# Performance work log

Measured on AMD Instinct MI355X. Metric: run time of the kernel, lower is better.

## Reference

```python
import jax, jax.numpy as jnp
import numpy as np

WINDOW = 32


def _dilate(mask, iters=5):
    # scipy binary_dilation with default cross structure, `iters` iterations
    m = mask.copy()
    for _ in range(iters):
        d = m.copy()
        d[1:, :] |= m[:-1, :]
        d[:-1, :] |= m[1:, :]
        d[:, 1:] |= m[:, :-1]
        d[:, :-1] |= m[:, 1:]
        m = d
    return m


def _label8(mask):
    # skimage measure.label, default 8-connectivity, via min-label propagation
    h, w = mask.shape
    lab = np.where(mask, np.arange(1, mask.size + 1, dtype=np.int64).reshape(h, w), 0)
    BIG = mask.size + 2
    while True:
        p = np.pad(np.where(mask, lab, BIG), 1, constant_values=BIG)
        m = np.full((h, w), BIG, dtype=np.int64)
        for dy in (-1, 0, 1):
            for dx in (-1, 0, 1):
                m = np.minimum(m, p[1 + dy:1 + dy + h, 1 + dx:1 + dx + w])
        new = np.where(mask, m, 0)
        if np.array_equal(new, lab):
            break
        lab = new
    u = np.unique(lab)
    out = np.searchsorted(u, lab)
    if u[0] != 0:
        out = out + 1
    return out


def _malis(seg_flat, e1, e2, costs, pos):
    # MALIS edge weights: Kruskal on descending affinities with union-find;
    # pos=True counts same-(nonzero)-label pairs merged by each edge,
    # pos=False counts cross-label pairs between labeled nodes.
    n = seg_flat.size
    parent = np.arange(n)
    cnt = [dict() for _ in range(n)]
    for i in range(n):
        s = int(seg_flat[i])
        if s != 0:
            cnt[i][s] = 1
    w = np.zeros(costs.shape[0], np.float32)

    def find(x):
        r = x
        while parent[r] != r:
            r = parent[r]
        while parent[x] != r:
            parent[x], x = r, parent[x]
        return r

    order = np.argsort(-costs, kind='stable')
    for ei in order:
        ra, rb = find(int(e1[ei])), find(int(e2[ei]))
        if ra == rb:
            continue
        ca, cb = cnt[ra], cnt[rb]
        small, large = (ca, cb) if len(ca) <= len(cb) else (cb, ca)
        same = 0
        for kk, v in small.items():
            same += v * large.get(kk, 0)
        if pos:
            w[ei] = same
        else:
            sa = sum(ca.values())
            sb = sum(cb.values())
            w[ei] = sa * sb - same
        parent[rb] = ra
        for kk, v in cb.items():
            ca[kk] = ca.get(kk, 0) + v
        cnt[rb] = None
    return w


def compute_malis_weights(pred_np, target_np):
    B, C, H, W = pred_np.shape
    wn_full = np.zeros(pred_np.shape, np.float32)
    wp_full = np.zeros(pred_np.shape, np.float32)
    win = WINDOW
    idx = np.arange(win * win).reshape(win, win)
    e1 = np.concatenate([idx[:, :-1].ravel(), idx[:-1, :].ravel()])
    e2 = np.concatenate([idx[:, 1:].ravel(), idx[1:, :].ravel()])
    for k in range(H // win):
        for j in range(W // win):
            p = pred_np[:, :, k * win:(k + 1) * win, j * win:(j + 1) * win]
            t = target_np[:, :, k * win:(k + 1) * win, j * win:(j + 1) * win]
            costs = np.concatenate([
                (p[:, :, :, :-1] + p[:, :, :, 1:]).reshape(B, -1),
                (p[:, :, :-1, :] + p[:, :, 1:, :]).reshape(B, -1)], axis=1).astype(np.float32)
            gtc = np.concatenate([
                (t[:, :, :, :-1] + t[:, :, :, 1:]).reshape(B, -1),
                (t[:, :, :-1, :] + t[:, :, 1:, :]).reshape(B, -1)], axis=1).astype(np.float32)
            costs_n = costs.copy()
            costs_p = costs.copy()
            costs_n[gtc > 20] = 20
            costs_p[gtc < 10] = 0
            gtc = np.minimum(gtc, 20)
            for i in range(B):
                sg = _label8(_dilate(t[i, 0] == 0, 5) == 0)
                en = _malis(sg.ravel(), e1, e2, costs_n[i], False)
                ep = _malis(sg.ravel(), e1, e2, costs_p[i], True)
                sn = en.sum()
                if sn > 0:
                    en = en / sn
                sp = ep.sum()
                if sp > 0:
                    ep = ep / sp
                en[gtc[i] >= 10] = 0
                ep[gtc[i] < 20] = 0
                for ew, out in ((en, wn_full), (ep, wp_full)):
                    wh, wv = np.split(ew, 2)
                    wh = wh.reshape(win, win - 1)
                    wv = wv.reshape(win - 1, win)
                    nodes = np.zeros((win, win), np.float32)
                    nodes[:, :-1] += wh
                    nodes[:, 1:] += wh
                    nodes[:-1, :] += wv
                    nodes[1:, :] += wv
                    out[i, 0, k * win:(k + 1) * win, j * win:(j + 1) * win] = nodes
    return wn_full, wp_full


def setup_inputs() -> dict:
    key = jax.random.key(0)
    k1, k2 = jax.random.split(key)
    pred = jax.random.uniform(k1, (2, 1, 256, 256), jnp.float32) * 20.0
    target = jax.random.randint(k2, (2, 1, 256, 256), 0, 26).astype(jnp.float32)
    return {"pred": pred, "target": target, "malis_lr": 1.0, "malis_lr_pos": 1.0}


def reference(pred, target, malis_lr, malis_lr_pos):
    # weights are computed from detached values (CPU graph algorithm), constants wrt autodiff
    wn, wp = compute_malis_weights(np.asarray(pred), np.asarray(target))
    wn = jnp.asarray(wn, jnp.float32)
    wp = jnp.asarray(wp, jnp.float32)
    loss = malis_lr * jnp.square(pred) * wn + malis_lr_pos * jnp.square(20.0 - pred) * wp
    return loss.sum()
```

## Files before the change

### kernel.cpp

```cpp
#include <hip/hip_runtime.h>
#include <cstdint>

#define NPIX  1024
#define NH    992
#define NEDGE 1984
#define NSORT 2048
#define NGRP  31
#define HFS   4300
#define POOLN (NPIX + 2*HFS)

typedef unsigned long long u64;
typedef unsigned int u32;

static __device__ __forceinline__ u64 packRoot(int sL,int off,int len,int cap){
    return (u64)(u32)(sL & 0x7FF) | ((u64)(u32)(off & 0x3FFF) << 11) |
           ((u64)(u32)(len & 0x7FF) << 25) | ((u64)(u32)(cap & 0x7FF) << 36);
}
#define R_SL(R)  ((int)((R) & 0x7FF))
#define R_OFF(R) ((int)(((R)>>11) & 0x3FFF))
#define R_LEN(R) ((int)(((R)>>25) & 0x7FF))
#define R_CAP(R) ((int)(((R)>>36) & 0x7FF))
#define EMASK 0x3FFFFFFu

static __device__ __forceinline__ int rdl(int v, int l){ return __builtin_amdgcn_readlane(v, l); }

static __device__ __forceinline__ u64 sxor64(u64 v, int m){
    u32 lo = (u32)__shfl_xor((int)(v & 0xFFFFFFFFull), m, 64);
    u32 hi = (u32)__shfl_xor((int)(v >> 32), m, 64);
    return ((u64)hi << 32) | lo;
}

static __device__ __forceinline__ void edgeAB(int e, int &a, int &b){
    if (e < NH) { int r = (int)((unsigned)e / 31u); a = e + r; b = a + 1; }
    else        { a = e - NH; b = a + 32; }
}

static __device__ __forceinline__ int winBase(int wslot){
    int bb = wslot >> 6;
    int win = wslot & 63;
    int wy = win >> 3, wx = win & 7;
    return bb * 65536 + (wy * 32) * 256 + wx * 32;
}

#define CE(x, y, up) { u64 _a=(x), _b=(y); bool _lt=(_a<_b); \
    u64 _mn=_lt?_a:_b, _mx=_lt?_b:_a; (x)=(up)?_mn:_mx; (y)=(up)?_mx:_mn; }
#define CEX(x, xm, keepmin) { u64 _p=sxor64((x),(xm)); bool _lt=((x)<_p); \
    u64 _mn=_lt?(x):_p, _mx=_lt?_p:(x); (x)=(keepmin)?_mn:_mx; }

static __device__ __forceinline__ int wredi(int v){
    #pragma unroll
    for (int o = 32; o > 0; o >>= 1) v += __shfl_xor(v, o, 64);
    return v;
}
static __device__ __forceinline__ float wredf(float v){
    #pragma unroll
    for (int o = 32; o > 0; o >>= 1) v += __shfl_xor(v, o, 64);
    return v;
}

__global__ __launch_bounds__(64) void malis_kernel(
    const float* __restrict__ pred,
    const float* __restrict__ target,
    const float* __restrict__ lr_p,
    const float* __restrict__ lrp_p,
    float* __restrict__ out)
{
    const int lane = threadIdx.x;
    const int bid  = blockIdx.x;
    const int ph   = bid & 1;
    const int wslot= bid >> 1;
    const int base = winBase(wslot);
    const u64 ltm = (1ull << lane) - 1;

    __shared__ __align__(16) u32 Ks_[NSORT];
    __shared__ u64   root_[NPIX];
    __shared__ u32   pool_[POOLN];
    __shared__ unsigned short Q_[NPIX];
    __shared__ float Qw_[NPIX];
    __shared__ u32   claim_[NPIX];
    __shared__ short par_[NPIX];
    __shared__ short H_[NPIX + 1];
    __shared__ float predL[NPIX];
    __shared__ float costs[NEDGE];
    __shared__ short seg[NPIX];
    __shared__ unsigned char tgtL[NPIX];
    __shared__ unsigned char gtcL[NEDGE];
    __shared__ u32   rowmaskL[32];
    __shared__ u32   fgL[32];
    __shared__ unsigned short baseL[33];

    u32* runPar = (u32*)pool_;
    unsigned short* labIdRun = (unsigned short*)(runPar + 512);

    for (int j = 0; j < 16; ++j) {
        int i = lane + 64 * j;
        int r = (j << 1) + (lane >> 5), c = lane & 31;
        float pv = pred[base + r * 256 + c];
        float tv = target[base + r * 256 + c];
        predL[i] = pv;
        tgtL[i]  = (unsigned char)tv;
        u64 zb = __ballot(tv == 0.0f);
        if (lane == 0) {
            rowmaskL[2*j]     = (u32)zb;
            rowmaskL[2*j + 1] = (u32)(zb >> 32);
        }
    }
    for (int x = lane; x < 512; x += 64) runPar[x] = (u32)x;
    __builtin_amdgcn_wave_barrier();

    if (lane < 32) {
        u32 m = rowmaskL[lane];
        #pragma unroll
        for (int it = 0; it < 5; ++it) {
            u32 um = __shfl(m, (lane == 0) ? 0 : lane - 1, 64);
            if (lane == 0) um = 0;
            u32 dm = __shfl(m, (lane == 31) ? 31 : lane + 1, 64);
            if (lane == 31) dm = 0;
            m = m | (m << 1) | (m >> 1) | um | dm;
        }
        u32 f = ~m;
        fgL[lane] = f;
        int ns = __popc(f & ~(f << 1));
        int x = ns;
        #pragma unroll
        for (int off = 1; off < 32; off <<= 1) {
            int y = __shfl(x, (lane >= off) ? lane - off : 0, 64);
            if (lane >= off) x += y;
        }
        baseL[lane] = (unsigned short)(x - ns);
        if (lane == 31) baseL[32] = (unsigned short)x;
    }
    __builtin_amdgcn_wave_barrier();
    const int nRuns = (int)baseL[32];

    for (;;) {
        bool chg = false;
        for (int j = 0; j < 16; ++j) {
            int i = lane + 64 * j;
            int r = i >> 5, c = i & 31;
            if (r == 0) continue;
            u32 fr = fgL[r];
            if (!((fr >> c) & 1u)) continue;
            u32 fu = fgL[r - 1];
            u32 nb = fu & (u32)((7ull << c) >> 1);
            if (!nb) continue;
            u32 Sr = fr & ~(fr << 1);
            int a = (int)baseL[r] + __popc(Sr & ((2u << c) - 1u)) - 1;
            for (;;) { int p = (int)runPar[a]; if (p == a) break; a = p; }
            u32 Su = fu & ~(fu << 1);
            int bu = (int)baseL[r - 1];
            while (nb) {
                int cc = __ffs((int)nb) - 1; nb &= nb - 1;
                int b = bu + __popc(Su & ((2u << cc) - 1u)) - 1;
                for (;;) { int p = (int)runPar[b]; if (p == b) break; b = p; }
                if (a != b) {
                    int mnr = a < b ? a : b;
                    int mxr = a ^ b ^ mnr;
                    atomicMin(&runPar[mxr], (u32)mnr);
                    chg = true;
                    a = mnr;
                }
            }
        }
        if (!__ballot(chg)) break;
        for (int x = lane; x < nRuns; x += 64) {
            u32 p = runPar[x];
            runPar[x] = runPar[p];
        }
        __builtin_amdgcn_wave_barrier();
    }

    {
        int kacc = 0;
        for (int x0 = 0; x0 < nRuns; x0 += 64) {
            int x = x0 + lane;
            bool isr = (x < nRuns) && ((int)runPar[x] == x);
            u64 bm = __ballot(isr);
            if (isr) labIdRun[x] = (unsigned short)(kacc + (int)__popcll(bm & ltm));
            kacc += (int)__popcll(bm);
        }
    }
    __builtin_amdgcn_wave_barrier();

    for (int j = 0; j < 16; ++j) {
        int i = lane + 64 * j;
        int r = i >> 5, c = i & 31;
        u32 fr = fgL[r];
        short s = 0;
        if ((fr >> c) & 1u) {
            u32 Sr = fr & ~(fr << 1);
            int x = (int)baseL[r] + __popc(Sr & ((2u << c) - 1u)) - 1;
            for (;;) { int p = (int)runPar[x]; if (p == x) break; x = p; }
            s = (short)((int)labIdRun[x] + 1);
        }
        seg[i] = s;
    }

    for (int e = lane; e < NEDGE; e += 64) {
        int a, b2; edgeAB(e, a, b2);
        costs[e] = predL[a] + predL[b2];
        gtcL[e]  = (unsigned char)(tgtL[a] + tgtL[b2]);
    }
    __builtin_amdgcn_wave_barrier();

    u64 sk[32];
    #pragma unroll
    for (int r = 0; r < 32; ++r) {
        int e = lane * 32 + r;
        u64 kv = ~0ULL;
        if (e < NEDGE) {
            float cv = costs[e];
            int g = gtcL[e];
            if (ph == 0) { if (g > 20) cv = 20.0f; }
            else         { if (g < 10) cv = 0.0f; }
            kv = (((u64)(~__float_as_uint(cv))) << 32) | (u32)e;
        }
        sk[r] = kv;
    }
    #pragma unroll
    for (int kk2 = 2; kk2 <= 32; kk2 <<= 1) {
        #pragma unroll
        for (int j = kk2 >> 1; j > 0; j >>= 1) {
            #pragma unroll
            for (int r = 0; r < 32; ++r) {
                if ((r & j) == 0) {
                    bool up = (kk2 == 32) ? ((lane & 1) == 0) : ((r & kk2) == 0);
                    CE(sk[r], sk[r | j], up);
                }
            }
        }
    }
    #pragma unroll
    for (int kk2 = 64; kk2 <= 2048; kk2 <<= 1) {
        const bool up = ((lane & (kk2 >> 5)) == 0);
        #pragma unroll
        for (int j = kk2 >> 1; j >= 32; j >>= 1) {
            const int xm = j >> 5;
            const bool keepmin = (((lane & xm) == 0) == up);
            #pragma unroll
            for (int r = 0; r < 32; ++r) { CEX(sk[r], xm, keepmin); }
        }
        #pragma unroll
        for (int j = 16; j > 0; j >>= 1) {
            #pragma unroll
            for (int r = 0; r < 32; ++r) {
                if ((r & j) == 0) { CE(sk[r], sk[r | j], up); }
            }
        }
    }
    #pragma unroll
    for (int r = 0; r < 32; r += 4) {
        uint4 v4;
        v4.x = (u32)sk[r]; v4.y = (u32)sk[r+1]; v4.z = (u32)sk[r+2]; v4.w = (u32)sk[r+3];
        *(uint4*)&Ks_[lane * 32 + r] = v4;
    }

    for (int i = lane; i < NPIX; i += 64) {
        short s2 = seg[i];
        par_[i] = (short)(i | (s2 ? 0x8000 : 0));
        root_[i] = s2 ? ((1ull << 62) | ((u32)(unsigned short)s2 << 16) | 1u) : 0ull;
        H_[i] = 0;
        claim_[i] = ~0u;
    }
    if (lane == 0) H_[NPIX] = 0;
    __builtin_amdgcn_wave_barrier();

    u32 bump = NPIX;
    u32 halfEnd = NPIX + HFS;
    int curHalf = 0;

    auto do_gc = [&]() {
        u32 tgt = (curHalf == 0) ? (u32)(NPIX + HFS) : (u32)NPIX;
        u32 nb = tgt;
        for (int c = 0; c < 16; ++c) {
            int i0 = c * 64 + lane;
            u64 Ri = root_[i0];
            bool live = (Ri != 0) && ((Ri >> 62) == 0);
            u64 rbm = __ballot(live);
            while (rbm) {
                int j = __ffsll(rbm) - 1; rbm &= rbm - 1;
                int r = c * 64 + j;
                u64 R = root_[r];
                int len = R_LEN(R);
                int off = R_OFF(R);
                for (int t = lane; t < len; t += 64) {
                    u32 v2 = pool_[off + t];
                    pool_[nb + t] = v2;
                }
                __builtin_amdgcn_wave_barrier();
                if (lane == 0) root_[r] = packRoot(R_SL(R), (int)nb, len, len);
                nb += (u32)len;
            }
        }
        bump = nb;
        halfEnd = tgt + HFS;
        curHalf ^= 1;
    };

    int qn = 0;
    u32 rnd = 1;
    int curE = (int)Ks_[lane];
    for (int g2 = 0; g2 < NGRP; ++g2) {
        int nextE = (g2 + 1 < NGRP) ? (int)Ks_[(g2 + 1) * 64 + lane] : 0;
        const int myE = curE;
        int ea, eb2; edgeAB(myE, ea, eb2);
        int ra = ea, rb = eb2;
        int laA, laB;
        for (;;) {
            int va = (int)(unsigned short)par_[ra];
            int vb = (int)(unsigned short)par_[rb];
            int pa = va & 0x3FF, pb = vb & 0x3FF;
            bool fa = (pa != ra), fb = (pb != rb);
            if (!fa && !fb) { laA = va >> 15; laB = vb >> 15; break; }
            int ga = (int)(unsigned short)par_[pa];
            int gb = (int)(unsigned short)par_[pb];
            if (fa) { par_[ra] = (short)ga; ra = ga & 0x3FF; }
            if (fb) { par_[rb] = (short)gb; rb = gb & 0x3FF; }
        }
        bool alive = (ra != rb);

        for (;;) {
            u64 aliveB = __ballot(alive);
            if (!aliveB) break;
            const bool av = alive;
            const bool solo = (aliveB & (aliveB - 1)) == 0;
            const u32 tag = ((0x03FFFFFFu - rnd) << 6) | (u32)lane;
            ++rnd;
            int mn = ra < rb ? ra : rb;
            int mx = ra ^ rb ^ mn;
            int winner = (laA == laB) ? mn : (laA ? ra : rb);
            int loser  = (laA == laB) ? mx : (laA ? rb : ra);
            bool wgt = (laA & laB) != 0;

            u64 RW = 0, RL = 0;
            if (av && wgt) { RW = root_[mn]; RL = root_[mx]; }

            u64 wgtB = __ballot(av && wgt);
            bool goW = false;
            if (wgtB) {
                if (solo) {
                    goW = av && wgt;
                } else {
                    if (av && wgt) { atomicMin(&claim_[loser], tag);
                                     atomicMin(&claim_[winner], tag); }
                    if (av && wgt) {
                        u32 cl = claim_[loser];
                        u32 cw = claim_[winner];
                        goW = (cl == tag) && (cw == tag);
                    }
                }
            }
            if (av && !wgt) par_[loser] = (short)winner;
            if (goW)        par_[loser] = (short)winner;

            u64 wm = __ballot(goW);
            int qidx = qn + (int)__popcll(wm & ltm);
            qn += (int)__popcll(wm);

            bool needPool = false;
            if (goW) {
                int tW = (int)(RW >> 62), tL2 = (int)(RL >> 62);
                if (tW != 0 && tL2 != 0) {
                    u32 a0 = (u32)RW & EMASK, a1 = (u32)(RW >> 26) & EMASK;
                    u32 b0 = (u32)RL & EMASK, b1 = (u32)(RL >> 26) & EMASK;
                    u32 la0 = a0 >> 16, la1 = a1 >> 16;
                    u32 lb0 = b0 >> 16, lb1 = b1 >> 16;
                    int ca0 = (int)(a0 & 0xFFFF), ca1 = (int)(a1 & 0xFFFF);
                    int cb0 = (int)(b0 & 0xFFFF), cb1 = (int)(b1 & 0xFFFF);
                    int sLa = ca0 + ((tW == 2) ? ca1 : 0);
                    int sLb = cb0 + ((tL2 == 2) ? cb1 : 0);
                    int same = 0;
                    if (lb0 == la0) same += ca0 * cb0;
                    else if (tW == 2 && lb0 == la1) same += ca1 * cb0;
                    if (tL2 == 2) {
                        if (lb1 == la0) same += ca0 * cb1;
                        else if (tW == 2 && lb1 == la1) same += ca1 * cb1;
                    }
                    u32 r0 = a0, r1 = (tW == 2) ? a1 : 0;
                    int n = tW; bool ovf = false;
                    if (lb0 == la0) r0 += (u32)cb0;
                    else if (tW == 2 && lb0 == la1) r1 += (u32)cb0;
                    else { if (n == 1) { r1 = b0; n = 2; } else ovf = true; }
                    if (tL2 == 2) {
                        if (lb1 == la0) r0 += (u32)cb1;
                        else if (tW == 2 && lb1 == la1) r1 += (u32)cb1;
                        else { if (n == 1) { r1 = b1; n = 2; } else ovf = true; }
                    }
                    if (!ovf) {
                        root_[mn] = ((u64)(u32)n << 62) | ((u64)r1 << 26) | r0;
                        root_[mx] = 0;
                        Qw_[qidx] = (float)(ph ? same : (sLa * sLb - same));
                        Q_[qidx]  = (unsigned short)myE;
                    } else needPool = true;
                } else needPool = true;
            }

            u64 pm = __ballot(needPool);
            while (pm) {
                int f = __ffsll(pm) - 1; pm &= pm - 1;
                int A  = rdl(mn, f),  B  = rdl(mx, f);
                int e  = rdl(myE, f), qi = rdl(qidx, f);
                u64 RA = root_[A], RB = root_[B];
                int tA = (int)(RA >> 62), tB = (int)(RB >> 62);
                int lenA = tA ? tA : R_LEN(RA);
                int lenB = tB ? tB : R_LEN(RB);
                if (bump + (u32)(lenA + lenB + 8) > halfEnd) {
                    do_gc();
                    RA = root_[A]; RB = root_[B];
                    tA = (int)(RA >> 62); tB = (int)(RB >> 62);
                    lenA = tA ? tA : R_LEN(RA);
                    lenB = tB ? tB : R_LEN(RB);
                }
                int sLa, sLb;
                int offA = 0, capA = 0, offB = 0, capB = 0;
                if (tA == 0) { sLa = R_SL(RA); offA = R_OFF(RA); capA = R_CAP(RA); }
                else {
                    u32 a0 = (u32)RA & EMASK, a1 = (u32)(RA >> 26) & EMASK;
                    sLa = (int)(a0 & 0xFFFF) + ((tA == 2) ? (int)(a1 & 0xFFFF) : 0);
                }
                if (tB == 0) { sLb = R_SL(RB); offB = R_OFF(RB); capB = R_CAP(RB); }
                else {
                    u32 b0 = (u32)RB & EMASK, b1 = (u32)(RB >> 26) & EMASK;
                    sLb = (int)(b0 & 0xFFFF) + ((tB == 2) ? (int)(b1 & 0xFFFF) : 0);
                }
                u32 eA = 0, eB = 0;
                if (lenA <= 64) {
                    if (tA == 0) { if (lane < lenA) eA = pool_[offA + lane]; }
                    else {
                        u32 a0 = (u32)RA & EMASK, a1 = (u32)(RA >> 26) & EMASK;
                        eA = (lane == 0) ? a0 : ((lane == 1 && tA == 2) ? a1 : 0);
                    }
                }
                if (lenB <= 64) {
                    if (tB == 0) { if (lane < lenB) eB = pool_[offB + lane]; }
                    else {
                        u32 b0 = (u32)RB & EMASK, b1 = (u32)(RB >> 26) & EMASK;
                        eB = (lane == 0) ? b0 : ((lane == 1 && tB == 2) ? b1 : 0);
                    }
                }
                u32 eS, eL; int lenS, lenL, offS, offL, capL, tL;
                if (lenA <= lenB) { eS=eA; lenS=lenA; offS=offA; eL=eB; lenL=lenB; offL=offB; capL=capB; tL=tB; }
                else              { eS=eB; lenS=lenB; offS=offB; eL=eA; lenL=lenA; offL=offA; capL=capA; tL=tA; }
                int dOff, dLen, dCap;
                int same = 0;
                u64 newR;

                if (lenS + lenL <= 64) {
                    dLen = lenL;
                    for (int t = 0; t < lenS; ++t) {
                        u32 xs = (u32)rdl((int)eS, t);
                        bool match = (lane < lenL) && ((eL >> 16) == (xs >> 16));
                        u64 mb = __ballot(match);
                        if (mb) {
                            int ml = __ffsll(mb) - 1;
                            same += (int)(xs & 0xFFFF) * ((int)rdl((int)eL, ml) & 0xFFFF);
                            if (match) eL += (xs & 0xFFFF);
                        } else {
                            if (lane == dLen) eL = xs;
                            dLen++;
                        }
                    }
                    if (dLen <= 2) {
                        u32 m0 = (u32)rdl((int)eL, 0) & EMASK;
                        u32 m1 = (dLen > 1) ? ((u32)rdl((int)eL, 1) & EMASK) : 0u;
                        newR = ((u64)(u32)dLen << 62) | ((u64)m1 << 26) | m0;
                    } else {
                        if (tL == 0 && dLen <= capL) { dOff = offL; dCap = capL; }
                        else { dOff = (int)bump; dCap = (dLen + 3) & ~3; bump += (u32)dCap; }
                        if (lane < dLen) pool_[dOff + lane] = eL;
                        newR = packRoot(sLa + sLb, dOff, dLen, dCap);
                    }
                } else {
                    dOff = (int)bump;
                    dCap = (lenL + lenS + 4) & ~3; bump += (u32)dCap;
                    if (lenS <= 64) {
                        if (lane < lenS) H_[eS >> 16] = (short)(eS & 0xFFFF);
                    } else {
                        for (int j = lane; j < lenS; j += 64) {
                            u32 es = pool_[offS + j];
                            H_[es >> 16] = (short)(es & 0xFFFF);
                        }
                    }
                    __builtin_amdgcn_wave_barrier();
                    int sp = 0;
                    for (int j = lane; j < lenL; j += 64) {
                        u32 el = pool_[offL + j];
                        int h = (int)H_[el >> 16];
                        sp += h * (int)(el & 0xFFFF);
                        pool_[dOff + j] = el + (u32)h;
                        if (h) H_[el >> 16] = 0;
                    }
                    same = wredi(sp);
                    __builtin_amdgcn_wave_barrier();
                    int baseU = 0;
                    if (lenS <= 64) {
                        bool un = (lane < lenS) && (H_[eS >> 16] != 0);
                        u64 ub = __ballot(un);
                        if (un) {
                            int pos = __popcll(ub & ltm);
                            pool_[dOff + lenL + pos] = eS;
                            H_[eS >> 16] = 0;
                        }
                        baseU = (int)__popcll(ub);
                    } else {
                        for (int j0 = 0; j0 < lenS; j0 += 64) {
                            int j = j0 + lane;
                            bool un = false; u32 es = 0;
                            if (j < lenS) { es = pool_[offS + j]; un = (H_[es >> 16] != 0); }
                            u64 ub = __ballot(un);
                            if (un) {
                                int pos = __popcll(ub & ltm);
                                pool_[dOff + lenL + baseU + pos] = es;
                                H_[es >> 16] = 0;
                            }
                            baseU += (int)__popcll(ub);
                        }
                    }
                    dLen = lenL + baseU;
                    newR = packRoot(sLa + sLb, dOff, dLen, dCap);
                }
                if (lane == 0) {
                    Qw_[qi] = (float)(ph ? same : (sLa * sLb - same));
                    Q_[qi]  = (unsigned short)e;
                    root_[A] = newR;
                    root_[B] = 0;
                }
                __builtin_amdgcn_wave_barrier();
            }

            if (av) {
                for (;;) {
                    int va = (int)(unsigned short)par_[ra];
                    int vb = (int)(unsigned short)par_[rb];
                    int pa = va & 0x3FF, pb = vb & 0x3FF;
                    bool fa = (pa != ra), fb = (pb != rb);
                    if (!fa && !fb) { laA = va >> 15; laB = vb >> 15; break; }
                    int ga = (int)(unsigned short)par_[pa];
                    int gb = (int)(unsigned short)par_[pb];
                    if (fa) { par_[ra] = (short)ga; ra = ga & 0x3FF; }
                    if (fb) { par_[rb] = (short)gb; rb = gb & 0x3FF; }
                }
                alive = (ra != rb);
            }
        }
        curE = nextE;
        __builtin_amdgcn_wave_barrier();
    }

    float s_loc = 0.0f;
    for (int q = lane; q < qn; q += 64) s_loc += Qw_[q];
    const float sn = wredf(s_loc);

    const float scale = ph ? lrp_p[0] : lr_p[0];
    float acc = 0.0f;
    for (int q = lane; q < qn; q += 64) {
        float wv2 = Qw_[q];
        if (wv2 == 0.0f) continue;
        if (sn > 0.0f) wv2 /= sn;
        int me = (int)Q_[q];
        int g = gtcL[me];
        bool zero = ph ? (g < 20) : (g >= 10);
        if (zero) continue;
        int a2, b2; edgeAB(me, a2, b2);
        float pa = predL[a2], pb = predL[b2];
        float fa2, fb2;
        if (ph == 0) { fa2 = pa * pa; fb2 = pb * pb; }
        else { float qa = 20.0f - pa, qb = 20.0f - pb; fa2 = qa * qa; fb2 = qb * qb; }
        acc += scale * wv2 * (fa2 + fb2);
    }
    acc = wredf(acc);
    if (lane == 0) atomicAdd(out, acc);
}

__global__ void zero_out_kernel(float* o)
{
    if (threadIdx.x == 0 && blockIdx.x == 0) o[0] = 0.0f;
}

extern "C" void kernel_launch(void* const* d_in, const int* in_sizes, int n_in,
                              void* d_out, int out_size, void* d_ws, size_t ws_size,
                              hipStream_t stream)
{
    const float* pred   = (const float*)d_in[0];
    const float* target = (const float*)d_in[1];
    const float* lr     = (const float*)d_in[2];
    const float* lrp    = (const float*)d_in[3];
    float* out = (float*)d_out;

    zero_out_kernel<<<1, 64, 0, stream>>>(out);
    malis_kernel<<<256, 64, 0, stream>>>(pred, target, lr, lrp, out);
}
```

Measured before the change: 356.7 us.

## Replace per-group lockstep union loop with per-lane streaming edge queues

```diff
diff --git a/kernel.cpp b/kernel.cpp
--- a/kernel.cpp
+++ b/kernel.cpp
@@ -299,252 +299,262 @@
 
     int qn = 0;
     u32 rnd = 1;
+    int gi = 0;
     int curE = (int)Ks_[lane];
-    for (int g2 = 0; g2 < NGRP; ++g2) {
-        int nextE = (g2 + 1 < NGRP) ? (int)Ks_[(g2 + 1) * 64 + lane] : 0;
-        const int myE = curE;
-        int ea, eb2; edgeAB(myE, ea, eb2);
-        int ra = ea, rb = eb2;
-        int laA, laB;
-        for (;;) {
-            int va = (int)(unsigned short)par_[ra];
-            int vb = (int)(unsigned short)par_[rb];
-            int pa = va & 0x3FF, pb = vb & 0x3FF;
-            bool fa = (pa != ra), fb = (pb != rb);
-            if (!fa && !fb) { laA = va >> 15; laB = vb >> 15; break; }
-            int ga = (int)(unsigned short)par_[pa];
-            int gb = (int)(unsigned short)par_[pb];
-            if (fa) { par_[ra] = (short)ga; ra = ga & 0x3FF; }
-            if (fb) { par_[rb] = (short)gb; rb = gb & 0x3FF; }
-        }
-        bool alive = (ra != rb);
-
-        for (;;) {
-            u64 aliveB = __ballot(alive);
-            if (!aliveB) break;
-            const bool av = alive;
-            const bool solo = (aliveB & (aliveB - 1)) == 0;
-            const u32 tag = ((0x03FFFFFFu - rnd) << 6) | (u32)lane;
-            ++rnd;
-            int mn = ra < rb ? ra : rb;
-            int mx = ra ^ rb ^ mn;
-            int winner = (laA == laB) ? mn : (laA ? ra : rb);
-            int loser  = (laA == laB) ? mx : (laA ? rb : ra);
-            bool wgt = (laA & laB) != 0;
-
-            u64 RW = 0, RL = 0;
-            if (av && wgt) { RW = root_[mn]; RL = root_[mx]; }
-
-            u64 wgtB = __ballot(av && wgt);
-            bool goW = false;
-            if (wgtB) {
-                if (solo) {
-                    goW = av && wgt;
-                } else {
-                    if (av && wgt) { atomicMin(&claim_[loser], tag);
-                                     atomicMin(&claim_[winner], tag); }
-                    if (av && wgt) {
-                        u32 cl = claim_[loser];
-                        u32 cw = claim_[winner];
-                        goW = (cl == tag) && (cw == tag);
-                    }
-                }
-            }
-            if (av && !wgt) par_[loser] = (short)winner;
-            if (goW)        par_[loser] = (short)winner;
-
-            u64 wm = __ballot(goW);
-            int qidx = qn + (int)__popcll(wm & ltm);
-            qn += (int)__popcll(wm);
-
-            bool needPool = false;
-            if (goW) {
-                int tW = (int)(RW >> 62), tL2 = (int)(RL >> 62);
-                if (tW != 0 && tL2 != 0) {
-                    u32 a0 = (u32)RW & EMASK, a1 = (u32)(RW >> 26) & EMASK;
-                    u32 b0 = (u32)RL & EMASK, b1 = (u32)(RL >> 26) & EMASK;
-                    u32 la0 = a0 >> 16, la1 = a1 >> 16;
-                    u32 lb0 = b0 >> 16, lb1 = b1 >> 16;
-                    int ca0 = (int)(a0 & 0xFFFF), ca1 = (int)(a1 & 0xFFFF);
-                    int cb0 = (int)(b0 & 0xFFFF), cb1 = (int)(b1 & 0xFFFF);
-                    int sLa = ca0 + ((tW == 2) ? ca1 : 0);
-                    int sLb = cb0 + ((tL2 == 2) ? cb1 : 0);
-                    int same = 0;
-                    if (lb0 == la0) same += ca0 * cb0;
-                    else if (tW == 2 && lb0 == la1) same += ca1 * cb0;
-                    if (tL2 == 2) {
-                        if (lb1 == la0) same += ca0 * cb1;
-                        else if (tW == 2 && lb1 == la1) same += ca1 * cb1;
-                    }
-                    u32 r0 = a0, r1 = (tW == 2) ? a1 : 0;
-                    int n = tW; bool ovf = false;
-                    if (lb0 == la0) r0 += (u32)cb0;
-                    else if (tW == 2 && lb0 == la1) r1 += (u32)cb0;
-                    else { if (n == 1) { r1 = b0; n = 2; } else ovf = true; }
-                    if (tL2 == 2) {
-                        if (lb1 == la0) r0 += (u32)cb1;
-                        else if (tW == 2 && lb1 == la1) r1 += (u32)cb1;
-                        else { if (n == 1) { r1 = b1; n = 2; } else ovf = true; }
-                    }
-                    if (!ovf) {
-                        root_[mn] = ((u64)(u32)n << 62) | ((u64)r1 << 26) | r0;
-                        root_[mx] = 0;
-                        Qw_[qidx] = (float)(ph ? same : (sLa * sLb - same));
-                        Q_[qidx]  = (unsigned short)myE;
-                    } else needPool = true;
+    int nextE = (int)Ks_[64 + lane];
+    bool have = true;
+
+    for (;;) {
+        if (!__ballot(have)) break;
+        ++rnd;
+        if (rnd > 100000u) break;
+        const u32 tagBase = (0x001FFFFFu - rnd) << 11;
+
+        int ra = 0, rb = 0, laA = 0, laB = 0;
+        if (have) {
+            int ea, eb2; edgeAB(curE, ea, eb2);
+            ra = ea; rb = eb2;
+            for (;;) {
+                int va = (int)(unsigned short)par_[ra];
+                int vb = (int)(unsigned short)par_[rb];
+                int pa = va & 0x3FF, pb = vb & 0x3FF;
+                bool fa = (pa != ra), fb = (pb != rb);
+                if (!fa && !fb) { laA = va >> 15; laB = vb >> 15; break; }
+                int ga2 = (int)(unsigned short)par_[pa];
+                int gb2 = (int)(unsigned short)par_[pb];
+                if (fa) { par_[ra] = (short)ga2; ra = ga2 & 0x3FF; }
+                if (fb) { par_[rb] = (short)gb2; rb = gb2 & 0x3FF; }
+            }
+        }
+        const bool dead  = have && (ra == rb);
+        const bool liveE = have && !dead;
+        const bool wgt   = liveE && (laA & laB);
+        const bool mixd  = liveE && (laA ^ laB);
+        const bool plmb  = liveE && !(laA | laB);
+
+        const int rank = gi * 64 + lane;
+        u32 mr = have ? (u32)rank : 0x7FFFFFFFu;
+        #pragma unroll
+        for (int o = 32; o; o >>= 1) {
+            u32 p = (u32)__shfl_xor((int)mr, o, 64);
+            mr = mr < p ? mr : p;
+        }
+        const bool gateOK = ((u32)rank < mr + 64u);
+
+        const int mn = ra < rb ? ra : rb;
+        const int mx = ra ^ rb ^ mn;
+        const int winner = (wgt || plmb) ? mn : (laA ? ra : rb);
+        const int loser  = (wgt || plmb) ? mx : (laA ? rb : ra);
+
+        u64 RW = 0, RL = 0;
+        if (wgt) { RW = root_[mn]; RL = root_[mx]; }
+
+        const u32 tag = tagBase | (u32)rank;
+        if (wgt) { atomicMin(&claim_[loser], tag); atomicMin(&claim_[winner], tag); }
+        bool goW = false;
+        if (wgt && gateOK) goW = (claim_[loser] == tag) && (claim_[winner] == tag);
+
+        if (plmb || (mixd && gateOK) || goW) par_[loser] = (short)winner;
+
+        u64 wm = __ballot(goW);
+        int qidx = qn + (int)__popcll(wm & ltm);
+        qn += (int)__popcll(wm);
+
+        bool needPool = false;
+        if (goW) {
+            int tW = (int)(RW >> 62), tL2 = (int)(RL >> 62);
+            if (tW != 0 && tL2 != 0) {
+                u32 a0 = (u32)RW & EMASK, a1 = (u32)(RW >> 26) & EMASK;
+                u32 b0 = (u32)RL & EMASK, b1 = (u32)(RL >> 26) & EMASK;
+                u32 la0 = a0 >> 16, la1 = a1 >> 16;
+                u32 lb0 = b0 >> 16, lb1 = b1 >> 16;
+                int ca0 = (int)(a0 & 0xFFFF), ca1 = (int)(a1 & 0xFFFF);
+                int cb0 = (int)(b0 & 0xFFFF), cb1 = (int)(b1 & 0xFFFF);
+                int sLa = ca0 + ((tW == 2) ? ca1 : 0);
+                int sLb = cb0 + ((tL2 == 2) ? cb1 : 0);
+                int same = 0;
+                if (lb0 == la0) same += ca0 * cb0;
+                else if (tW == 2 && lb0 == la1) same += ca1 * cb0;
+                if (tL2 == 2) {
+                    if (lb1 == la0) same += ca0 * cb1;
+                    else if (tW == 2 && lb1 == la1) same += ca1 * cb1;
+                }
+                u32 r0 = a0, r1 = (tW == 2) ? a1 : 0;
+                int n = tW; bool ovf = false;
+                if (lb0 == la0) r0 += (u32)cb0;
+                else if (tW == 2 && lb0 == la1) r1 += (u32)cb0;
+                else { if (n == 1) { r1 = b0; n = 2; } else ovf = true; }
+                if (tL2 == 2) {
+                    if (lb1 == la0) r0 += (u32)cb1;
+                    else if (tW == 2 && lb1 == la1) r1 += (u32)cb1;
+                    else { if (n == 1) { r1 = b1; n = 2; } else ovf = true; }
+                }
+                if (!ovf) {
+                    root_[mn] = ((u64)(u32)n << 62) | ((u64)r1 << 26) | r0;
+                    root_[mx] = 0;
+                    Qw_[qidx] = (float)(ph ? same : (sLa * sLb - same));
+                    Q_[qidx]  = (unsigned short)curE;
                 } else needPool = true;
-            }
-
-            u64 pm = __ballot(needPool);
-            while (pm) {
-                int f = __ffsll(pm) - 1; pm &= pm - 1;
-                int A  = rdl(mn, f),  B  = rdl(mx, f);
-                int e  = rdl(myE, f), qi = rdl(qidx, f);
-                u64 RA = root_[A], RB = root_[B];
-                int tA = (int)(RA >> 62), tB = (int)(RB >> 62);
-                int lenA = tA ? tA : R_LEN(RA);
-                int lenB = tB ? tB : R_LEN(RB);
-                if (bump + (u32)(lenA + lenB + 8) > halfEnd) {
-                    do_gc();
-                    RA = root_[A]; RB = root_[B];
-                    tA = (int)(RA >> 62); tB = (int)(RB >> 62);
-                    lenA = tA ? tA : R_LEN(RA);
-                    lenB = tB ? tB : R_LEN(RB);
-                }
-                int sLa, sLb;
-                int offA = 0, capA = 0, offB = 0, capB = 0;
-                if (tA == 0) { sLa = R_SL(RA); offA = R_OFF(RA); capA = R_CAP(RA); }
+            } else needPool = true;
+        }
+
+        u64 pm = __ballot(needPool);
+        while (pm) {
+            int f = __ffsll(pm) - 1; pm &= pm - 1;
+            int A  = rdl(mn, f),  B  = rdl(mx, f);
+            int e  = rdl(curE, f), qi = rdl(qidx, f);
+            u64 RA = root_[A], RB = root_[B];
+            int tA = (int)(RA >> 62), tB = (int)(RB >> 62);
+            int lenA = tA ? tA : R_LEN(RA);
+            int lenB = tB ? tB : R_LEN(RB);
+            if (bump + (u32)(lenA + lenB + 8) > halfEnd) {
+                do_gc();
+                RA = root_[A]; RB = root_[B];
+                tA = (int)(RA >> 62); tB = (int)(RB >> 62);
+                lenA = tA ? tA : R_LEN(RA);
+                lenB = tB ? tB : R_LEN(RB);
+            }
+            int sLa, sLb;
+            int offA = 0, capA = 0, offB = 0, capB = 0;
+            if (tA == 0) { sLa = R_SL(RA); offA = R_OFF(RA); capA = R_CAP(RA); }
+            else {
+                u32 a0 = (u32)RA & EMASK, a1 = (u32)(RA >> 26) & EMASK;
+                sLa = (int)(a0 & 0xFFFF) + ((tA == 2) ? (int)(a1 & 0xFFFF) : 0);
+            }
+            if (tB == 0) { sLb = R_SL(RB); offB = R_OFF(RB); capB = R_CAP(RB); }
+            else {
+                u32 b0 = (u32)RB & EMASK, b1 = (u32)(RB >> 26) & EMASK;
+                sLb = (int)(b0 & 0xFFFF) + ((tB == 2) ? (int)(b1 & 0xFFFF) : 0);
+            }
+            u32 eA = 0, eB = 0;
+            if (lenA <= 64) {
+                if (tA == 0) { if (lane < lenA) eA = pool_[offA + lane]; }
                 else {
                     u32 a0 = (u32)RA & EMASK, a1 = (u32)(RA >> 26) & EMASK;
-                    sLa = (int)(a0 & 0xFFFF) + ((tA == 2) ? (int)(a1 & 0xFFFF) : 0);
-                }
-                if (tB == 0) { sLb = R_SL(RB); offB = R_OFF(RB); capB = R_CAP(RB); }
+                    eA = (lane == 0) ? a0 : ((lane == 1 && tA == 2) ? a1 : 0);
+                }
+            }
+            if (lenB <= 64) {
+                if (tB == 0) { if (lane < lenB) eB = pool_[offB + lane]; }
                 else {
                     u32 b0 = (u32)RB & EMASK, b1 = (u32)(RB >> 26) & EMASK;
-                    sLb = (int)(b0 & 0xFFFF) + ((tB == 2) ? (int)(b1 & 0xFFFF) : 0);
-                }
-                u32 eA = 0, eB = 0;
-                if (lenA <= 64) {
-                    if (tA == 0) { if (lane < lenA) eA = pool_[offA + lane]; }
-                    else {
-                        u32 a0 = (u32)RA & EMASK, a1 = (u32)(RA >> 26) & EMASK;
-                        eA = (lane == 0) ? a0 : ((lane == 1 && tA == 2) ? a1 : 0);
+                    eB = (lane == 0) ? b0 : ((lane == 1 && tB == 2) ? b1 : 0);
+                }
+            }
+            u32 eS, eL; int lenS, lenL, offS, offL, capL, tL;
+            if (lenA <= lenB) { eS=eA; lenS=lenA; offS=offA; eL=eB; lenL=lenB; offL=offB; capL=capB; tL=tB; }
+            else              { eS=eB; lenS=lenB; offS=offB; eL=eA; lenL=lenA; offL=offA; capL=capA; tL=tA; }
+            int dOff, dLen, dCap;
+            int same = 0;
+            u64 newR;
+
+            if (lenS + lenL <= 64) {
+                dLen = lenL;
+                for (int t = 0; t < lenS; ++t) {
+                    u32 xs = (u32)rdl((int)eS, t);
+                    bool match = (lane < lenL) && ((eL >> 16) == (xs >> 16));
+                    u64 mb = __ballot(match);
+                    if (mb) {
+                        int ml = __ffsll(mb) - 1;
+                        same += (int)(xs & 0xFFFF) * ((int)rdl((int)eL, ml) & 0xFFFF);
+                        if (match) eL += (xs & 0xFFFF);
+                    } else {
+                        if (lane == dLen) eL = xs;
+                        dLen++;
                     }
                 }
-                if (lenB <= 64) {
-                    if (tB == 0) { if (lane < lenB) eB = pool_[offB + lane]; }
-                    else {
-                        u32 b0 = (u32)RB & EMASK, b1 = (u32)(RB >> 26) & EMASK;
-                        eB = (lane == 0) ? b0 : ((lane == 1 && tB == 2) ? b1 : 0);
+                if (dLen <= 2) {
+                    u32 m0 = (u32)rdl((int)eL, 0) & EMASK;
+                    u32 m1 = (dLen > 1) ? ((u32)rdl((int)eL, 1) & EMASK) : 0u;
+                    newR = ((u64)(u32)dLen << 62) | ((u64)m1 << 26) | m0;
+                } else {
+                    if (tL == 0 && dLen <= capL) { dOff = offL; dCap = capL; }
+                    else { dOff = (int)bump; dCap = (dLen + 3) & ~3; bump += (u32)dCap; }
+                    if (lane < dLen) pool_[dOff + lane] = eL;
+                    newR = packRoot(sLa + sLb, dOff, dLen, dCap);
+                }
+            } else {
+                dOff = (int)bump;
+                dCap = (lenL + lenS + 4) & ~3; bump += (u32)dCap;
+                if (lenS <= 64) {
+                    if (lane < lenS) H_[eS >> 16] = (short)(eS & 0xFFFF);
+                } else {
+                    for (int j = lane; j < lenS; j += 64) {
+                        u32 es = pool_[offS + j];
+                        H_[es >> 16] = (short)(es & 0xFFFF);
                     }
                 }
-                u32 eS, eL; int lenS, lenL, offS, offL, capL, tL;
-                if (lenA <= lenB) { eS=eA; lenS=lenA; offS=offA; eL=eB; lenL=lenB; offL=offB; capL=capB; tL=tB; }
-                else              { eS=eB; lenS=lenB; offS=offB; eL=eA; lenL=lenA; offL=offA; capL=capA; tL=tA; }
-                int dOff, dLen, dCap;
-                int same = 0;
-                u64 newR;
-
-                if (lenS + lenL <= 64) {
-                    dLen = lenL;
-                    for (int t = 0; t < lenS; ++t) {
-                        u32 xs = (u32)rdl((int)eS, t);
-                        bool match = (lane < lenL) && ((eL >> 16) == (xs >> 16));
-                        u64 mb = __ballot(match);
-                        if (mb) {
-                            int ml = __ffsll(mb) - 1;
-                            same += (int)(xs & 0xFFFF) * ((int)rdl((int)eL, ml) & 0xFFFF);
-                            if (match) eL += (xs & 0xFFFF);
-                        } else {
-                            if (lane == dLen) eL = xs;
-                            dLen++;
-                        }
+                __builtin_amdgcn_wave_barrier();
+                int sp = 0;
+                for (int j = lane; j < lenL; j += 64) {
+                    u32 el = pool_[offL + j];
+                    int h = (int)H_[el >> 16];
+                    sp += h * (int)(el & 0xFFFF);
+                    pool_[dOff + j] = el + (u32)h;
+                    if (h) H_[el >> 16] = 0;
+                }
+                same = wredi(sp);
+                __builtin_amdgcn_wave_barrier();
+                int baseU = 0;
+                if (lenS <= 64) {
+                    bool un = (lane < lenS) && (H_[eS >> 16] != 0);
+                    u64 ub = __ballot(un);
+                    if (un) {
+                        int pos = __popcll(ub & ltm);
+                        pool_[dOff + lenL + pos] = eS;
+                        H_[eS >> 16] = 0;
                     }
-                    if (dLen <= 2) {
-                        u32 m0 = (u32)rdl((int)eL, 0) & EMASK;
-                        u32 m1 = (dLen > 1) ? ((u32)rdl((int)eL, 1) & EMASK) : 0u;
-                        newR = ((u64)(u32)dLen << 62) | ((u64)m1 << 26) | m0;
-                    } else {
-                        if (tL == 0 && dLen <= capL) { dOff = offL; dCap = capL; }
-                        else { dOff = (int)bump; dCap = (dLen + 3) & ~3; bump += (u32)dCap; }
-                        if (lane < dLen) pool_[dOff + lane] = eL;
-                        newR = packRoot(sLa + sLb, dOff, dLen, dCap);
-                    }
+                    baseU = (int)__popcll(ub);
                 } else {
-                    dOff = (int)bump;
-                    dCap = (lenL + lenS + 4) & ~3; bump += (u32)dCap;
-                    if (lenS <= 64) {
-                        if (lane < lenS) H_[eS >> 16] = (short)(eS & 0xFFFF);
-                    } else {
-                        for (int j = lane; j < lenS; j += 64) {
-                            u32 es = pool_[offS + j];
-                            H_[es >> 16] = (short)(es & 0xFFFF);
-                        }
-                    }
-                    __builtin_amdgcn_wave_barrier();
-                    int sp = 0;
-                    for (int j = lane; j < lenL; j += 64) {
-                        u32 el = pool_[offL + j];
-                        int h = (int)H_[el >> 16];
-                        sp += h * (int)(el & 0xFFFF);
-                        pool_[dOff + j] = el + (u32)h;
-                        if (h) H_[el >> 16] = 0;
-                    }
-                    same = wredi(sp);
-                    __builtin_amdgcn_wave_barrier();
-                    int baseU = 0;
-                    if (lenS <= 64) {
-                        bool un = (lane < lenS) && (H_[eS >> 16] != 0);
+                    for (int j0 = 0; j0 < lenS; j0 += 64) {
+                        int j = j0 + lane;
+                        bool un = false; u32 es = 0;
+                        if (j < lenS) { es = pool_[offS + j]; un = (H_[es >> 16] != 0); }
                         u64 ub = __ballot(un);
                         if (un) {
                             int pos = __popcll(ub & ltm);
-                            pool_[dOff + lenL + pos] = eS;
-                            H_[eS >> 16] = 0;
+                            pool_[dOff + lenL + baseU + pos] = es;
+                            H_[es >> 16] = 0;
                         }
-                        baseU = (int)__popcll(ub);
-                    } else {
-                        for (int j0 = 0; j0 < lenS; j0 += 64) {
-                            int j = j0 + lane;
-                            bool un = false; u32 es = 0;
-                            if (j < lenS) { es = pool_[offS + j]; un = (H_[es >> 16] != 0); }
-                            u64 ub = __ballot(un);
-                            if (un) {
-                                int pos = __popcll(ub & ltm);
-                                pool_[dOff + lenL + baseU + pos] = es;
-                                H_[es >> 16] = 0;
-                            }
-                            baseU += (int)__popcll(ub);
-                        }
+                        baseU += (int)__popcll(ub);
                     }
-                    dLen = lenL + baseU;
-                    newR = packRoot(sLa + sLb, dOff, dLen, dCap);
-                }
-                if (lane == 0) {
-                    Qw_[qi] = (float)(ph ? same : (sLa * sLb - same));
-                    Q_[qi]  = (unsigned short)e;
-                    root_[A] = newR;
-                    root_[B] = 0;
-                }
-                __builtin_amdgcn_wave_barrier();
-            }
-
-            if (av) {
-                for (;;) {
-                    int va = (int)(unsigned short)par_[ra];
-                    int vb = (int)(unsigned short)par_[rb];
-                    int pa = va & 0x3FF, pb = vb & 0x3FF;
-                    bool fa = (pa != ra), fb = (pb != rb);
-                    if (!fa && !fb) { laA = va >> 15; laB = vb >> 15; break; }
-                    int ga = (int)(unsigned short)par_[pa];
-                    int gb = (int)(unsigned short)par_[pb];
-                    if (fa) { par_[ra] = (short)ga; ra = ga & 0x3FF; }
-                    if (fb) { par_[rb] = (short)gb; rb = gb & 0x3FF; }
-                }
-                alive = (ra != rb);
-            }
-        }
-        curE = nextE;
-        __builtin_amdgcn_wave_barrier();
+                }
+                dLen = lenL + baseU;
+                newR = packRoot(sLa + sLb, dOff, dLen, dCap);
+            }
+            if (lane == 0) {
+                Qw_[qi] = (float)(ph ? same : (sLa * sLb - same));
+                Q_[qi]  = (unsigned short)e;
+                root_[A] = newR;
+                root_[B] = 0;
+            }
+            __builtin_amdgcn_wave_barrier();
+        }
+
+        bool retired = dead || goW;
+        if (liveE && !goW) {
+            int x = ra, y = rb;
+            for (;;) {
+                int va = (int)(unsigned short)par_[x];
+                int vb = (int)(unsigned short)par_[y];
+                int pa = va & 0x3FF, pb = vb & 0x3FF;
+                bool fa = (pa != x), fb = (pb != y);
+                if (!fa && !fb) break;
+                int ga2 = (int)(unsigned short)par_[pa];
+                int gb2 = (int)(unsigned short)par_[pb];
+                if (fa) { par_[x] = (short)ga2; x = ga2 & 0x3FF; }
+                if (fb) { par_[y] = (short)gb2; y = gb2 & 0x3FF; }
+            }
+            if (x == y) retired = true;
+        }
+        if (have && retired) {
+            ++gi;
+            if (gi >= NGRP) have = false;
+            else {
+                curE = nextE;
+                if (gi + 1 < NGRP) nextE = (int)Ks_[(gi + 1) * 64 + lane];
+            }
+        }
     }
 
     float s_loc = 0.0f;
```

After: 396.4 us. 11.1% more time.

## Arbitrate all concurrent unions via claims and relink roots with wave broadcasts

Applied to the files above, without the earlier changes.

```diff
diff --git a/kernel.cpp b/kernel.cpp
--- a/kernel.cpp
+++ b/kernel.cpp
@@ -331,31 +331,28 @@
             int winner = (laA == laB) ? mn : (laA ? ra : rb);
             int loser  = (laA == laB) ? mx : (laA ? rb : ra);
             bool wgt = (laA & laB) != 0;
+            int labW = laA | laB;
 
             u64 RW = 0, RL = 0;
             if (av && wgt) { RW = root_[mn]; RL = root_[mx]; }
 
-            u64 wgtB = __ballot(av && wgt);
-            bool goW = false;
-            if (wgtB) {
-                if (solo) {
-                    goW = av && wgt;
-                } else {
-                    if (av && wgt) { atomicMin(&claim_[loser], tag);
-                                     atomicMin(&claim_[winner], tag); }
-                    if (av && wgt) {
-                        u32 cl = claim_[loser];
-                        u32 cw = claim_[winner];
-                        goW = (cl == tag) && (cw == tag);
-                    }
-                }
-            }
-            if (av && !wgt) par_[loser] = (short)winner;
-            if (goW)        par_[loser] = (short)winner;
-
+            bool go = false;
+            if (solo) {
+                go = av;
+            } else {
+                if (av)        atomicMin(&claim_[loser],  tag);
+                if (av && wgt) atomicMin(&claim_[winner], tag);
+                if (av) {
+                    u32 cl = claim_[loser];
+                    u32 cw = wgt ? claim_[winner] : tag;
+                    go = (cl == tag) && (cw == tag);
+                }
+            }
+            bool goW = go && wgt;
             u64 wm = __ballot(goW);
             int qidx = qn + (int)__popcll(wm & ltm);
             qn += (int)__popcll(wm);
+            if (go) par_[loser] = (short)winner;
 
             bool needPool = false;
             if (goW) {
@@ -528,20 +525,23 @@
                 __builtin_amdgcn_wave_barrier();
             }
 
-            if (av) {
-                for (;;) {
-                    int va = (int)(unsigned short)par_[ra];
-                    int vb = (int)(unsigned short)par_[rb];
-                    int pa = va & 0x3FF, pb = vb & 0x3FF;
-                    bool fa = (pa != ra), fb = (pb != rb);
-                    if (!fa && !fb) { laA = va >> 15; laB = vb >> 15; break; }
-                    int ga = (int)(unsigned short)par_[pa];
-                    int gb = (int)(unsigned short)par_[pb];
-                    if (fa) { par_[ra] = (short)ga; ra = ga & 0x3FF; }
-                    if (fb) { par_[rb] = (short)gb; rb = gb & 0x3FF; }
-                }
-                alive = (ra != rb);
-            }
+            u64 subB = __ballot(go);
+            for (int pass = 0; pass < 64; ++pass) {
+                bool chg = false;
+                u64 t = subB;
+                while (t) {
+                    int f = __ffsll(t) - 1; t &= t - 1;
+                    int Lf = rdl(loser,  f);
+                    int Wf = rdl(winner, f);
+                    int lw = rdl(labW,   f);
+                    if (av) {
+                        if (ra == Lf) { ra = Wf; laA = lw; chg = true; }
+                        if (rb == Lf) { rb = Wf; laB = lw; chg = true; }
+                    }
+                }
+                if (!__ballot(chg)) break;
+            }
+            if (av) alive = (ra != rb);
         }
         curE = nextE;
         __builtin_amdgcn_wave_barrier();
```

Measured after the change: 997.8 us. 2.8x slower.
